# Optimization experiments

Hardware: AMD Instinct MI355X
Metric: run time of the kernel (lower is better)

## Reference

```python
import jax, jax.numpy as jnp
import numpy as np
import math

N, C, W = 4, 768, 2048
H = 12            # num_attention_heads
D = C // H        # attention_head_size = 64
G = 4             # q/k/v groups


def grouped_conv1x1(x, w, b):
    # x: [N, C, W]; w: [G, C/G, C/G] (cout_per_g, cin_per_g); b: [C]
    xg = x.reshape(N, G, C // G, W)
    out = jnp.einsum('goc,ngcw->ngow', w, xg)       # [N, G, C/G, W]
    return out.reshape(N, C, W) + b[None, :, None]


def setup_inputs() -> dict:
    key = jax.random.key(0)
    ks = jax.random.split(key, 7)
    s = 1.0 / math.sqrt(C // G)
    return {
        'hidden_states': jax.random.normal(ks[0], (N, C, W), jnp.float32),
        'attention_mask': jnp.zeros((N, 1, 1, W), jnp.float32),
        'wq': jax.random.normal(ks[1], (G, C // G, C // G), jnp.float32) * s,
        'bq': jax.random.normal(ks[2], (C,), jnp.float32) * 0.02,
        'wk': jax.random.normal(ks[3], (G, C // G, C // G), jnp.float32) * s,
        'bk': jax.random.normal(ks[4], (C,), jnp.float32) * 0.02,
        'wv': jax.random.normal(ks[5], (G, C // G, C // G), jnp.float32) * s,
        'bv': jax.random.normal(ks[6], (C,), jnp.float32) * 0.02,
    }


def reference(hidden_states, attention_mask, wq, bq, wk, bk, wv, bv):
    q = grouped_conv1x1(hidden_states, wq, bq)       # [N, C, W]
    k = grouped_conv1x1(hidden_states, wk, bk)
    v = grouped_conv1x1(hidden_states, wv, bv)
    # transpose_for_scores_conv1d: [N,C,W] -> [N,H,W,D]
    q = q.reshape(N, H, D, W).transpose(0, 1, 3, 2)
    # transpose_key_for_scores_conv1d: [N,C,W] -> [N,H,D,W]
    k = k.reshape(N, H, D, W)
    v = v.reshape(N, H, D, W).transpose(0, 1, 3, 2)
    scores = jnp.einsum('nhqd,nhdk->nhqk', q, k) / math.sqrt(D)
    scores = scores + attention_mask                 # broadcast [N,1,1,W]
    probs = jax.nn.softmax(scores, axis=-1)          # dropout p=0 (eval)
    ctx = jnp.einsum('nhqk,nhkd->nhqd', probs, v)    # [N,H,W,D]
    # transpose_output_conv1d: [N,H,W,D] -> [N,C,W]
    return ctx.transpose(0, 1, 3, 2).reshape(N, C, W)
```

## Files before the change

### kernel.cpp

```cpp
#include <hip/hip_runtime.h>
#include <math.h>

typedef __attribute__((ext_vector_type(4))) float floatx4;
typedef __attribute__((ext_vector_type(8))) short shortx8;
typedef __attribute__((ext_vector_type(4))) short shortx4;

#define NB 4
#define CC 768
#define WW 2048
#define HH 12
#define DD 64
#define GG 4
#define CG 192
#define HPG 3
#define L2E 1.4426950408889634f
#define C18 0.18033688011112043f
#define MSH 11.541560327111707f
#define WSZ (GG * CG * CG)

__device__ __forceinline__ float fast_exp2(float x) {
    return __builtin_amdgcn_exp2f(x);
}

__device__ __forceinline__ short f2bf(float f) {
    union { float f; unsigned u; } v; v.f = f;
    unsigned r = v.u + 0x7fffu + ((v.u >> 16) & 1u);
    return (short)(r >> 16);
}

template<int CTRL>
__device__ __forceinline__ float dppror(float v) {
    return __int_as_float(__builtin_amdgcn_update_dpp(
        0, __float_as_int(v), CTRL, 0xf, 0xf, false));
}
__device__ __forceinline__ float rsum16(float v) {
    v += dppror<0x128>(v);
    v += dppror<0x124>(v);
    v += dppror<0x122>(v);
    v += dppror<0x121>(v);
    return v;
}

__device__ __forceinline__ void gl_lds16(const void* g, void* l) {
    __builtin_amdgcn_global_load_lds(
        (const __attribute__((address_space(1))) unsigned int*)g,
        (__attribute__((address_space(3))) unsigned int*)l, 16, 0, 0);
}

__global__ __launch_bounds__(256) void prep(
    const float* __restrict__ x,
    const float* __restrict__ wq, const float* __restrict__ wk,
    const float* __restrict__ wv,
    short* __restrict__ XTh, short* __restrict__ Wf)
{
    __shared__ short Th[64 * 72];
    const int tid = threadIdx.x;
    const int b   = blockIdx.x;

    if (b < 1536) {
        const int w0 = (b & 31) * 64;
        const int c0 = ((b >> 5) % 12) * 64;
        const int n  = b / 384;
        const int w  = tid & 63;
        const int cb = (tid >> 6) * 16;

        float xv[16];
        #pragma unroll
        for (int j = 0; j < 16; ++j)
            xv[j] = x[((size_t)n * CC + c0 + cb + j) * WW + w0 + w];

        shortx8 hi0, hi1;
        #pragma unroll
        for (int j = 0; j < 8; ++j) { hi0[j] = f2bf(xv[j]); hi1[j] = f2bf(xv[j + 8]); }
        *(shortx8*)&Th[w * 72 + cb]     = hi0;
        *(shortx8*)&Th[w * 72 + cb + 8] = hi1;
        __syncthreads();

        const int wr = tid >> 2;
        const int cc = (tid & 3) * 16;
        const size_t ro = ((size_t)n * WW + w0 + wr) * CC + c0 + cc;
        *(shortx8*)&XTh[ro]     = *(const shortx8*)&Th[wr * 72 + cc];
        *(shortx8*)&XTh[ro + 8] = *(const shortx8*)&Th[wr * 72 + cc + 8];
    } else {
        const int t = (b - 1536) * 256 + tid;
        const int g  = t / (CG * CG);
        const int r  = t - g * (CG * CG);
        const int o  = r / CG;
        const int k  = r - o * CG;
        const int off = (((g * 12 + (o >> 4)) * 6 + (k >> 5)) * 512)
                      + ((k >> 3) & 3) * 128 + (o & 15) * 8 + (k & 7);
        const float* src[3] = {wq, wk, wv};
        #pragma unroll
        for (int m = 0; m < 3; ++m)
            Wf[m * WSZ + off] = f2bf(src[m][t]);
    }
}

__global__ __launch_bounds__(256) void qkv_gemm(
    const short* __restrict__ XTh, const short* __restrict__ Wf,
    const float* __restrict__ bq, const float* __restrict__ bk,
    const float* __restrict__ bv,
    short* __restrict__ Qb, short* __restrict__ Kb, short* __restrict__ Vb)
{
    __shared__ __align__(16) char smem[26112];
    short* Xh_l = (short*)smem;

    const int lin  = blockIdx.x;
    const int xcd  = lin & 7;
    const int iw   = lin >> 3;
    const int mat  = iw % 3;
    const int tile = (iw / 3) * 8 + xcd;
    const int p0   = (tile & 31) * 64;
    const int g    = (tile >> 5) & 3;
    const int n    = tile >> 7;

    const int tid  = threadIdx.x;
    const int wid  = __builtin_amdgcn_readfirstlane(tid >> 6);
    const int lane = tid & 63;
    const int l15  = lane & 15;
    const int quad = lane >> 4;
    const int ob   = wid * 48;

    {
        const short* xhb = XTh + ((size_t)n * WW + p0) * CC + g * CG;
        #pragma unroll
        for (int rd = 0; rd < 6; ++rd) {
            const int Lb = rd * 256 + wid * 64;
            const int L  = Lb + lane;
            const int p  = (L * 2731) >> 16;
            const int sc = L - p * 24;
            const int ss = (sc & ~7) | ((sc & 7) ^ (p & 7));
            gl_lds16(xhb + (size_t)p * CC + ss * 8, &Xh_l[Lb * 8]);
        }
    }
    __syncthreads();

    floatx4 acc[3][4];
    #pragma unroll
    for (int mi = 0; mi < 3; ++mi)
        #pragma unroll
        for (int ni = 0; ni < 4; ++ni) acc[mi][ni] = (floatx4)0.0f;

    const short* wfm = Wf + (size_t)mat * WSZ + lane * 8;

    #pragma unroll
    for (int ks = 0; ks < 6; ++ks) {
        shortx8 ah[3], bh[4];
        #pragma unroll
        for (int mi = 0; mi < 3; ++mi)
            ah[mi] = *(const shortx8*)(wfm + (((g * 12 + wid * 3 + mi) * 6 + ks) << 9));
        #pragma unroll
        for (int ni = 0; ni < 4; ++ni) {
            const int p  = ni * 16 + l15;
            const int vp = (ks >> 1) * 8 + ((((ks & 1) * 4) + quad) ^ (p & 7));
            bh[ni] = *(const shortx8*)&Xh_l[(p * 24 + vp) * 8];
        }
        #pragma unroll
        for (int mi = 0; mi < 3; ++mi)
            #pragma unroll
            for (int ni = 0; ni < 4; ++ni)
                acc[mi][ni] = __builtin_amdgcn_mfma_f32_16x16x32_bf16(ah[mi], bh[ni], acc[mi][ni], 0, 0, 0);
    }

    const float* bias = (mat == 0) ? bq : (mat == 1) ? bk : bv;
    short* Y = (mat == 0) ? Qb : (mat == 1) ? Kb : Vb;

    __syncthreads();

    if (mat < 2) {
        short* T = (short*)smem;
        #pragma unroll
        for (int mi = 0; mi < 3; ++mi) {
            float4 b4 = *(const float4*)&bias[g * CG + ob + mi * 16 + quad * 4];
            const int o = ob + mi * 16 + quad * 4;
            #pragma unroll
            for (int ni = 0; ni < 4; ++ni) {
                const int p = ni * 16 + l15;
                T[p * 200 + o]     = f2bf(acc[mi][ni][0] + b4.x);
                T[p * 200 + o + 1] = f2bf(acc[mi][ni][1] + b4.y);
                T[p * 200 + o + 2] = f2bf(acc[mi][ni][2] + b4.z);
                T[p * 200 + o + 3] = f2bf(acc[mi][ni][3] + b4.w);
            }
        }
        __syncthreads();
        #pragma unroll
        for (int hc = 0; hc < HPG; ++hc) {
            const size_t nh = (size_t)n * HH + g * HPG + hc;
            #pragma unroll
            for (int half = 0; half < 2; ++half) {
                const int idx = tid + half * 256;
                const int p  = idx >> 3;
                const int dc = (idx & 7) * 8;
                *(shortx8*)&Y[(nh * WW + p0 + p) * DD + dc] =
                    *(const shortx8*)&T[p * 200 + hc * 64 + dc];
            }
        }
    } else {
        short* T = (short*)smem;
        #pragma unroll
        for (int mi = 0; mi < 3; ++mi) {
            float4 b4 = *(const float4*)&bias[g * CG + ob + mi * 16 + quad * 4];
            const int o = ob + mi * 16 + quad * 4;
            #pragma unroll
            for (int ni = 0; ni < 4; ++ni) {
                const int p = ni * 16 + l15;
                T[(o)     * 68 + p] = f2bf(acc[mi][ni][0] + b4.x);
                T[(o + 1) * 68 + p] = f2bf(acc[mi][ni][1] + b4.y);
                T[(o + 2) * 68 + p] = f2bf(acc[mi][ni][2] + b4.z);
                T[(o + 3) * 68 + p] = f2bf(acc[mi][ni][3] + b4.w);
            }
        }
        __syncthreads();
        #pragma unroll
        for (int pass = 0; pass < 6; ++pass) {
            const int idx = tid + pass * 256;
            const int o  = idx >> 3;
            const int pc = (idx & 7) * 8;
            const size_t nh = (size_t)n * HH + g * HPG + (o >> 6);
            const int d = o & 63;
            *(shortx8*)&Y[(nh * DD + d) * WW + p0 + pc] =
                *(const shortx8*)&T[o * 68 + pc];
        }
    }
}

#define PST 72
#define RST 65

__global__ __launch_bounds__(256) void attn_split(
    const short* __restrict__ Qb, const short* __restrict__ Kb,
    const short* __restrict__ Vb, const float* __restrict__ mask,
    float* __restrict__ out)
{
    __shared__ __align__(16) char smem[50176];
    short* Pl = (short*)(smem + 32768);
    float* Ml = (float*)(smem + 41984);

    const int lin  = blockIdx.x;
    const int xcd  = lin & 7;
    const int slot = lin >> 3;
    const int pair = xcd * 6 + (slot >> 5);
    const int qt   = slot & 31;
    const int n    = pair / HH;
    const int h    = pair % HH;
    const int q0   = qt * 64;

    const int tid  = threadIdx.x;
    const int wid  = __builtin_amdgcn_readfirstlane(tid >> 6);
    const int lane = tid & 63;
    const int l15  = lane & 15;
    const int quad = lane >> 4;

    const size_t nh = (size_t)n * HH + h;
    const short* Kbase = Kb + nh * WW * DD;
    const short* Vbase = Vb + nh * DD * WW;

    {
        const float* mbase = mask + (size_t)n * WW;
        #pragma unroll
        for (int i = 0; i < WW / 256; ++i)
            Ml[tid + i * 256] = fmaf(mbase[tid + i * 256], L2E, -MSH);
    }

    shortx8 qf[2];
    {
        const short* qp = Qb + (nh * WW + q0 + wid * 16 + l15) * DD + quad * 8;
        qf[0] = *(const shortx8*)(qp);
        qf[1] = *(const shortx8*)(qp + 32);
    }

    floatx4 oacc[4];
    #pragma unroll
    for (int nn2 = 0; nn2 < 4; ++nn2) oacc[nn2] = (floatx4)0.0f;
    float lst[4] = {0.f, 0.f, 0.f, 0.f};

    short* Pw = Pl + wid * 16 * PST;

    const int r0  = wid * 16 + (lane >> 3);
    const int r1  = r0 + 8;
    const int cg0 = (lane & 7) ^ (r0 & 7);
    const int cg1 = (lane & 7) ^ (r1 & 7);
    const short* kp0 = Kbase + (size_t)r0 * DD + cg0 * 8;
    const short* kp1 = Kbase + (size_t)r1 * DD + cg1 * 8;
    const short* vp0 = Vbase + (size_t)r0 * WW + cg0 * 8;
    const short* vp1 = Vbase + (size_t)r1 * WW + cg1 * 8;
    const int KR0 = (wid * 16) * 64, KR1 = (wid * 16 + 8) * 64;

    #define STAGE(j, bb)                                                      \
        do {                                                                  \
            short* ksd = (short*)(smem + (bb) * 8192);                        \
            short* vsd = (short*)(smem + 16384 + (bb) * 8192);                \
            gl_lds16(kp0 + (size_t)(j) * 64 * DD, ksd + KR0);                 \
            gl_lds16(kp1 + (size_t)(j) * 64 * DD, ksd + KR1);                 \
            gl_lds16(vp0 + (j) * 64, vsd + KR0);                              \
            gl_lds16(vp1 + (j) * 64, vsd + KR1);                              \
        } while (0)

    STAGE(0, 0);
    __syncthreads();

    for (int kt = 0; kt < WW / 64; ++kt) {
        const int bb = kt & 1;
        if (kt + 1 < WW / 64) STAGE(kt + 1, 1 - bb);

        const short* Ks_l = (const short*)(smem + bb * 8192);
        const short* Vs_l = (const short*)(smem + 16384 + bb * 8192);
        const int k0 = kt * 64;

        shortx8 kf[4][2], vf[4][2];
        #pragma unroll
        for (int jj = 0; jj < 4; ++jj) {
            const int r = 16 * jj + l15;
            #pragma unroll
            for (int hf = 0; hf < 2; ++hf)
                kf[jj][hf] = *(const shortx8*)&Ks_l[r * 64 + (((hf * 4 + quad) ^ (r & 7)) * 8)];
        }
        #pragma unroll
        for (int nn2 = 0; nn2 < 4; ++nn2) {
            const int r = 16 * nn2 + l15;
            #pragma unroll
            for (int hf = 0; hf < 2; ++hf)
                vf[nn2][hf] = *(const shortx8*)&Vs_l[r * 64 + (((hf * 4 + quad) ^ (r & 7)) * 8)];
        }
        float mv2[4];
        #pragma unroll
        for (int jj = 0; jj < 4; ++jj)
            mv2[jj] = Ml[k0 + 16 * jj + l15];

        floatx4 sacc[4];
        #pragma unroll
        for (int jj = 0; jj < 4; ++jj) {
            sacc[jj] = (floatx4)0.0f;
            sacc[jj] = __builtin_amdgcn_mfma_f32_16x16x32_bf16(qf[0], kf[jj][0], sacc[jj], 0, 0, 0);
            sacc[jj] = __builtin_amdgcn_mfma_f32_16x16x32_bf16(qf[1], kf[jj][1], sacc[jj], 0, 0, 0);
        }

        #pragma unroll
        for (int jj = 0; jj < 4; ++jj) {
            #pragma unroll
            for (int r = 0; r < 4; ++r) {
                float p = fast_exp2(fmaf(sacc[jj][r], C18, mv2[jj]));
                lst[r] += p;
                Pw[(quad * 4 + r) * PST + 16 * jj + l15] = f2bf(p);
            }
        }

        shortx8 pf0 = *(const shortx8*)&Pw[l15 * PST + quad * 8];
        shortx8 pf1 = *(const shortx8*)&Pw[l15 * PST + 32 + quad * 8];

        #pragma unroll
        for (int nn2 = 0; nn2 < 4; ++nn2) {
            oacc[nn2] = __builtin_amdgcn_mfma_f32_16x16x32_bf16(pf0, vf[nn2][0], oacc[nn2], 0, 0, 0);
            oacc[nn2] = __builtin_amdgcn_mfma_f32_16x16x32_bf16(pf1, vf[nn2][1], oacc[nn2], 0, 0, 0);
        }
        __syncthreads();
    }
    #undef STAGE

    float linv[4];
    #pragma unroll
    for (int r = 0; r < 4; ++r) linv[r] = 1.0f / rsum16(lst[r]);

    float* Ol = (float*)smem;
    #pragma unroll
    for (int nn2 = 0; nn2 < 4; ++nn2)
        #pragma unroll
        for (int r = 0; r < 4; ++r)
            Ol[(wid * 16 + quad * 4 + r) * RST + nn2 * 16 + l15] = oacc[nn2][r] * linv[r];
    __syncthreads();

    float* obase = out + (nh * DD) * WW + q0;
    #pragma unroll
    for (int it = 0; it < 4; ++it) {
        const int idx = tid + it * 256;
        const int q4 = (idx & 15) * 4;
        const int d  = idx >> 4;
        floatx4 v;
        #pragma unroll
        for (int i = 0; i < 4; ++i) v[i] = Ol[(q4 + i) * RST + d];
        *(floatx4*)&obase[(size_t)d * WW + q4] = v;
    }
}

extern "C" void kernel_launch(void* const* d_in, const int* in_sizes, int n_in,
                              void* d_out, int out_size, void* d_ws, size_t ws_size,
                              hipStream_t stream) {
    const float* x    = (const float*)d_in[0];
    const float* mask = (const float*)d_in[1];
    const float* wq   = (const float*)d_in[2];
    const float* bq   = (const float*)d_in[3];
    const float* wk   = (const float*)d_in[4];
    const float* bk   = (const float*)d_in[5];
    const float* wv   = (const float*)d_in[6];
    const float* bv   = (const float*)d_in[7];
    float* out = (float*)d_out;

    const size_t per = (size_t)NB * HH * WW * DD;
    short* Qb  = (short*)d_ws;
    short* Kb  = Qb + per;
    short* Vb  = Kb + per;
    short* XTh = Vb + per;
    short* Wfp = XTh + per;

    hipLaunchKernelGGL(prep, dim3(1536 + WSZ / 256), dim3(256), 0, stream,
                       x, wq, wk, wv, XTh, Wfp);
    hipLaunchKernelGGL(qkv_gemm, dim3(1536), dim3(256), 0, stream,
                       XTh, Wfp, bq, bk, bv, Qb, Kb, Vb);
    hipLaunchKernelGGL(attn_split, dim3(1536), dim3(256), 0, stream,
                       Qb, Kb, Vb, mask, out);
}
```

Before: 194.9 us.

## Swap MFMA operand order to compute transposed scores and simplify softmax stores

Swaps the A/B operands of both MFMAs so each lane holds four consecutive keys for a single query row, rather than four query rows for one key. Mask values then load as one float4, the bf16 probabilities are packed in pairs and written with a single 8-byte store, and the row sum needs only two cross-lane shuffles instead of per-row DPP reductions. The output accumulator comes out already transposed, so the staging tile is written in d-major order with stride 68 and read back as aligned float4 vectors. This is meant to cut VALU work, LDS store count and reduction overhead in the inner loop, at the risk of new LDS bank conflicts in the transposed staging writes.

Measured after the change: 196.6 us. Within noise of the previous version (+0.9%).

```diff
diff --git a/kernel.cpp b/kernel.cpp
--- a/kernel.cpp
+++ b/kernel.cpp
@@ -28,18 +28,20 @@
     return (short)(r >> 16);
 }
 
-template<int CTRL>
-__device__ __forceinline__ float dppror(float v) {
-    return __int_as_float(__builtin_amdgcn_update_dpp(
-        0, __float_as_int(v), CTRL, 0xf, 0xf, false));
-}
-__device__ __forceinline__ float rsum16(float v) {
-    v += dppror<0x128>(v);
-    v += dppror<0x124>(v);
-    v += dppror<0x122>(v);
-    v += dppror<0x121>(v);
-    return v;
-}
+__device__ __forceinline__ unsigned pack_bf16(float a, float b) {
+#if __has_builtin(__builtin_amdgcn_cvt_pk_bf16_f32)
+    typedef __bf16 bf16x2_t __attribute__((ext_vector_type(2)));
+    bf16x2_t p = __builtin_amdgcn_cvt_pk_bf16_f32(a, b);
+    return __builtin_bit_cast(unsigned, p);
+#else
+    union { float f; unsigned u; } x, y; x.f = a; y.f = b;
+    unsigned ra = (x.u + 0x7fffu + ((x.u >> 16) & 1u)) >> 16;
+    unsigned rb = (y.u + 0x7fffu + ((y.u >> 16) & 1u)) & 0xffff0000u;
+    return ra | rb;
+#endif
+}
+
+struct __align__(8) u2 { unsigned x, y; };
 
 __device__ __forceinline__ void gl_lds16(const void* g, void* l) {
     __builtin_amdgcn_global_load_lds(
@@ -225,7 +227,7 @@
 }
 
 #define PST 72
-#define RST 65
+#define RST 68
 
 __global__ __launch_bounds__(256) void attn_split(
     const short* __restrict__ Qb, const short* __restrict__ Kb,
@@ -272,7 +274,7 @@
     floatx4 oacc[4];
     #pragma unroll
     for (int nn2 = 0; nn2 < 4; ++nn2) oacc[nn2] = (floatx4)0.0f;
-    float lst[4] = {0.f, 0.f, 0.f, 0.f};
+    float lsumA = 0.f, lsumB = 0.f;
 
     short* Pw = Pl + wid * 16 * PST;
 
@@ -322,27 +324,26 @@
             for (int hf = 0; hf < 2; ++hf)
                 vf[nn2][hf] = *(const shortx8*)&Vs_l[r * 64 + (((hf * 4 + quad) ^ (r & 7)) * 8)];
         }
-        float mv2[4];
-        #pragma unroll
-        for (int jj = 0; jj < 4; ++jj)
-            mv2[jj] = Ml[k0 + 16 * jj + l15];
 
         floatx4 sacc[4];
         #pragma unroll
         for (int jj = 0; jj < 4; ++jj) {
             sacc[jj] = (floatx4)0.0f;
-            sacc[jj] = __builtin_amdgcn_mfma_f32_16x16x32_bf16(qf[0], kf[jj][0], sacc[jj], 0, 0, 0);
-            sacc[jj] = __builtin_amdgcn_mfma_f32_16x16x32_bf16(qf[1], kf[jj][1], sacc[jj], 0, 0, 0);
+            sacc[jj] = __builtin_amdgcn_mfma_f32_16x16x32_bf16(kf[jj][0], qf[0], sacc[jj], 0, 0, 0);
+            sacc[jj] = __builtin_amdgcn_mfma_f32_16x16x32_bf16(kf[jj][1], qf[1], sacc[jj], 0, 0, 0);
         }
 
         #pragma unroll
         for (int jj = 0; jj < 4; ++jj) {
-            #pragma unroll
-            for (int r = 0; r < 4; ++r) {
-                float p = fast_exp2(fmaf(sacc[jj][r], C18, mv2[jj]));
-                lst[r] += p;
-                Pw[(quad * 4 + r) * PST + 16 * jj + l15] = f2bf(p);
-            }
+            float4 mvv = *(const float4*)&Ml[k0 + 16 * jj + quad * 4];
+            float p0 = fast_exp2(fmaf(sacc[jj][0], C18, mvv.x));
+            float p1 = fast_exp2(fmaf(sacc[jj][1], C18, mvv.y));
+            float p2 = fast_exp2(fmaf(sacc[jj][2], C18, mvv.z));
+            float p3 = fast_exp2(fmaf(sacc[jj][3], C18, mvv.w));
+            lsumA += p0 + p1;
+            lsumB += p2 + p3;
+            u2 pk = { pack_bf16(p0, p1), pack_bf16(p2, p3) };
+            *(u2*)&Pw[l15 * PST + 16 * jj + quad * 4] = pk;
         }
 
         shortx8 pf0 = *(const shortx8*)&Pw[l15 * PST + quad * 8];
@@ -350,23 +351,24 @@
 
         #pragma unroll
         for (int nn2 = 0; nn2 < 4; ++nn2) {
-            oacc[nn2] = __builtin_amdgcn_mfma_f32_16x16x32_bf16(pf0, vf[nn2][0], oacc[nn2], 0, 0, 0);
-            oacc[nn2] = __builtin_amdgcn_mfma_f32_16x16x32_bf16(pf1, vf[nn2][1], oacc[nn2], 0, 0, 0);
+            oacc[nn2] = __builtin_amdgcn_mfma_f32_16x16x32_bf16(vf[nn2][0], pf0, oacc[nn2], 0, 0, 0);
+            oacc[nn2] = __builtin_amdgcn_mfma_f32_16x16x32_bf16(vf[nn2][1], pf1, oacc[nn2], 0, 0, 0);
         }
         __syncthreads();
     }
     #undef STAGE
 
-    float linv[4];
-    #pragma unroll
-    for (int r = 0; r < 4; ++r) linv[r] = 1.0f / rsum16(lst[r]);
+    float lsum = lsumA + lsumB;
+    lsum += __shfl_xor(lsum, 16);
+    lsum += __shfl_xor(lsum, 32);
+    const float linv = 1.0f / lsum;
 
     float* Ol = (float*)smem;
     #pragma unroll
     for (int nn2 = 0; nn2 < 4; ++nn2)
         #pragma unroll
         for (int r = 0; r < 4; ++r)
-            Ol[(wid * 16 + quad * 4 + r) * RST + nn2 * 16 + l15] = oacc[nn2][r] * linv[r];
+            Ol[(nn2 * 16 + quad * 4 + r) * RST + wid * 16 + l15] = oacc[nn2][r] * linv;
     __syncthreads();
 
     float* obase = out + (nh * DD) * WW + q0;
@@ -375,10 +377,7 @@
         const int idx = tid + it * 256;
         const int q4 = (idx & 15) * 4;
         const int d  = idx >> 4;
-        floatx4 v;
-        #pragma unroll
-        for (int i = 0; i < 4; ++i) v[i] = Ol[(q4 + i) * RST + d];
-        *(floatx4*)&obase[(size_t)d * WW + q4] = v;
+        *(floatx4*)&obase[(size_t)d * WW + q4] = *(const floatx4*)&Ol[d * RST + q4];
     }
 }
 
```
